# Kernel optimization log

Hardware: AMD Instinct MI355X
Metric: run time of the kernel (lower is better)

The kernel has to match this reference:

```python
import jax, jax.numpy as jnp
import numpy as np

W_DIM = 72  # positional_encoding(3 coords, 12 freqs) -> 3*12*2
_F1 = np.array([1.0, 3.0, 3.0, 1.0], dtype=np.float32)
_F2 = np.outer(_F1, _F1); _F2 = _F2 / _F2.sum()  # normalized StyleGAN resample filter


def upsample2x(x):
    """Antialiased 2x upsample: zero-insertion + 4-tap [1,3,3,1] FIR, gain=4 (upfirdn2d)."""
    C = x.shape[1]
    k = jnp.tile(jnp.asarray(_F2 * 4.0, x.dtype)[None, None], (C, 1, 1, 1))  # [C,1,4,4]
    return jax.lax.conv_general_dilated(
        x, k, (1, 1), ((2, 2), (2, 2)), lhs_dilation=(2, 2),
        feature_group_count=C, dimension_numbers=('NCHW', 'OIHW', 'NCHW'))


def affine(w_vec, aw, ab):
    # FullyConnectedLayer: runtime weight gain 1/sqrt(w_dim), bias init 1
    return (w_vec @ aw.T) / np.sqrt(W_DIM) + ab


def mod_conv(x, weight, styles, demodulate=True, padding=1):
    """StyleGAN2 modulated conv2d (batch=1). weight [Co,Ci,k,k], styles [Ci]."""
    w = weight * styles[None, :, None, None]
    if demodulate:
        d = jax.lax.rsqrt(jnp.sum(w * w, axis=(1, 2, 3)) + 1e-8)
        w = w * d[:, None, None, None]
    return jax.lax.conv_general_dilated(
        x, w, (1, 1), ((padding, padding), (padding, padding)),
        dimension_numbers=('NCHW', 'OIHW', 'NCHW'))


def syn_layer(x, w_vec, aw, ab, cw, cb, up):
    s = affine(w_vec, aw, ab)
    if up:
        x = upsample2x(x)
    x = mod_conv(x, cw, s, True, 1)
    # bias_act: lrelu, gain sqrt(2), conv_clamp 256 (noise_strength init 0 -> no noise)
    x = jax.nn.leaky_relu(x + cb[None, :, None, None], 0.2) * np.sqrt(2.0)
    return jnp.clip(x, -256.0, 256.0)


def to_rgb(x, w_vec, aw, ab, cw, cb):
    s = affine(w_vec, aw, ab) / np.sqrt(cw.shape[1])  # ToRGB weight_gain 1/sqrt(Cin)
    y = mod_conv(x, cw, s, False, 0)
    return jnp.clip(y + cb[None, :, None, None], -256.0, 256.0)


def reference(rays, rgbs, conv_w, conv_b, bn_gamma, bn_beta, bn_mean, bn_var,
              a0_w, a0_b, w0, b0, a1_w, a1_b, w1, b1, t0_aw, t0_ab, t0_w, t0_b,
              a2_w, a2_b, w2, b2, a3_w, a3_b, w3, b3, t1_aw, t1_ab, t1_w, t1_b):
    # style vector from positional encoding of ray origin
    p = rays[0, :3, 0, 0]
    fb = 2.0 ** jnp.arange(12, dtype=rays.dtype)
    pts = (p[:, None] * fb[None, :]).reshape(-1)  # (36,)
    w_vec = jnp.concatenate([jnp.sin(pts), jnp.cos(pts)])  # (72,)
    # mapping: 1x1 conv + relu + BatchNorm2d (eval-mode)
    feat = jnp.einsum('oi,bihw->bohw', conv_w[:, :, 0, 0], rgbs) + conv_b[None, :, None, None]
    feat = jax.nn.relu(feat)
    inv = jax.lax.rsqrt(bn_var + 1e-5)
    feat = (feat - bn_mean[None, :, None, None]) * (inv * bn_gamma)[None, :, None, None] + bn_beta[None, :, None, None]
    rgb = feat[:, :3]
    # block0: 32ch@128 -> 256ch@256, skip-architecture ToRGB
    x = syn_layer(feat, w_vec, a0_w, a0_b, w0, b0, True)
    x = syn_layer(x, w_vec, a1_w, a1_b, w1, b1, False)
    img = upsample2x(rgb) + to_rgb(x, w_vec, t0_aw, t0_ab, t0_w, t0_b)
    # block1: 256ch@256 -> 128ch@512
    x = syn_layer(x, w_vec, a2_w, a2_b, w2, b2, True)
    x = syn_layer(x, w_vec, a3_w, a3_b, w3, b3, False)
    img = upsample2x(img) + to_rgb(x, w_vec, t1_aw, t1_ab, t1_w, t1_b)
    return img  # [1,3,512,512]


def setup_inputs() -> dict:
    key = jax.random.key(0)
    ks = jax.random.split(key, 16)
    rn = lambda k, s: jax.random.normal(k, s, dtype=jnp.float32)
    z = lambda s: jnp.zeros(s, jnp.float32)
    o = lambda s: jnp.ones(s, jnp.float32)
    inp = {}
    inp['rays'] = rn(ks[0], (1, 6, 128, 128))
    inp['rgbs'] = jax.random.uniform(ks[1], (1, 3, 128, 128), dtype=jnp.float32)
    inp['conv_w'] = rn(ks[2], (32, 3, 1, 1)); inp['conv_b'] = z((32,))
    inp['bn_gamma'] = o((32,)); inp['bn_beta'] = z((32,))
    inp['bn_mean'] = z((32,)); inp['bn_var'] = o((32,))
    inp['a0_w'] = rn(ks[3], (32, 72)); inp['a0_b'] = o((32,))
    inp['w0'] = rn(ks[4], (256, 32, 3, 3)); inp['b0'] = z((256,))
    inp['a1_w'] = rn(ks[5], (256, 72)); inp['a1_b'] = o((256,))
    inp['w1'] = rn(ks[6], (256, 256, 3, 3)); inp['b1'] = z((256,))
    inp['t0_aw'] = rn(ks[7], (256, 72)); inp['t0_ab'] = o((256,))
    inp['t0_w'] = rn(ks[8], (3, 256, 1, 1)); inp['t0_b'] = z((3,))
    inp['a2_w'] = rn(ks[9], (256, 72)); inp['a2_b'] = o((256,))
    inp['w2'] = rn(ks[10], (128, 256, 3, 3)); inp['b2'] = z((128,))
    inp['a3_w'] = rn(ks[11], (128, 72)); inp['a3_b'] = o((128,))
    inp['w3'] = rn(ks[12], (128, 128, 3, 3)); inp['b3'] = z((128,))
    inp['t1_aw'] = rn(ks[13], (128, 72)); inp['t1_ab'] = o((128,))
    inp['t1_w'] = rn(ks[14], (3, 128, 1, 1)); inp['t1_b'] = z((3,))
    return inp
```

## Files before the change

### kernel.cpp

```cpp
#include <hip/hip_runtime.h>
#include <cstddef>

typedef __attribute__((ext_vector_type(8))) short short8;
typedef __attribute__((ext_vector_type(4))) float f32x4;
typedef __attribute__((address_space(3))) void lds_void;
typedef const __attribute__((address_space(1))) void glob_void;

static const size_t OFF_S0    = 0;
static const size_t OFF_S1    = 64;
static const size_t OFF_S2    = 320;
static const size_t OFF_S3    = 576;
static const size_t OFF_MT0   = 704;
static const size_t OFF_MT1   = 1472;
static const size_t OFF_ZERO  = 1856;
static const size_t OFF_RGBF  = 2048;
static const size_t OFF_IMG0  = 51200;
static const size_t OFF_RGBP  = 247808;
static const size_t OFF_WQ0   = 1900544;
static const size_t OFF_WQ1   = 1937408;
static const size_t OFF_WQ2   = 2232320;
static const size_t OFF_WQ3   = 2379776;
static const size_t OFF_FEAT  = 2453504;
static const size_t OFF_UFEAT = 2715648;
static const size_t OFF_X1    = 4194304;
static const size_t OFF_X2    = 4194304;
static const size_t OFF_U     = 20971520;
static const size_t OFF_X0    = 20971520;

__device__ __forceinline__ unsigned short f2bf(float f) {
  unsigned int u = __float_as_uint(f);
  return (unsigned short)((u + 0x7FFFu + ((u >> 16) & 1u)) >> 16);
}
__device__ __forceinline__ float b2f(short h) {
  return __uint_as_float(((unsigned int)(unsigned short)h) << 16);
}

__global__ void __launch_bounds__(256) prep_kernel(
    const float* __restrict__ rays,
    const float* __restrict__ a0w, const float* __restrict__ a0b,
    const float* __restrict__ a1w, const float* __restrict__ a1b,
    const float* __restrict__ t0aw, const float* __restrict__ t0ab,
    const float* __restrict__ a2w, const float* __restrict__ a2b,
    const float* __restrict__ a3w, const float* __restrict__ a3b,
    const float* __restrict__ t1aw, const float* __restrict__ t1ab,
    const float* __restrict__ t0w, const float* __restrict__ t1w,
    float* __restrict__ ws)
{
  __shared__ float wv[72];
  __shared__ float st0l[256];
  __shared__ float st1l[128];
  const int tid = threadIdx.x;
  if (tid < 128) ws[OFF_ZERO + tid] = 0.f;
  if (tid < 36) {
    int i = tid / 12, j = tid % 12;
    float v = rays[i * 16384] * (float)(1 << j);
    wv[tid]      = sinf(v);
    wv[36 + tid] = cosf(v);
  }
  __syncthreads();
  const float inv72 = 0.11785113019775793f;

  if (tid < 32) {
    float d = 0.f;
    for (int k = 0; k < 72; ++k) d += wv[k] * a0w[tid * 72 + k];
    ws[OFF_S0 + tid] = fmaf(d, inv72, a0b[tid]);
  }
  {
    float d = 0.f;
    for (int k = 0; k < 72; ++k) d += wv[k] * a1w[tid * 72 + k];
    ws[OFF_S1 + tid] = fmaf(d, inv72, a1b[tid]);
  }
  {
    float d = 0.f;
    for (int k = 0; k < 72; ++k) d += wv[k] * t0aw[tid * 72 + k];
    st0l[tid] = fmaf(d, inv72, t0ab[tid]) * 0.0625f;
  }
  {
    float d = 0.f;
    for (int k = 0; k < 72; ++k) d += wv[k] * a2w[tid * 72 + k];
    ws[OFF_S2 + tid] = fmaf(d, inv72, a2b[tid]);
  }
  if (tid < 128) {
    float d = 0.f;
    for (int k = 0; k < 72; ++k) d += wv[k] * a3w[tid * 72 + k];
    ws[OFF_S3 + tid] = fmaf(d, inv72, a3b[tid]);
  }
  if (tid < 128) {
    float d = 0.f;
    for (int k = 0; k < 72; ++k) d += wv[k] * t1aw[tid * 72 + k];
    st1l[tid] = fmaf(d, inv72, t1ab[tid]) * 0.08838834764831845f;
  }
  __syncthreads();
  for (int i = tid; i < 768; i += 256) ws[OFF_MT0 + i] = t0w[i] * st0l[i & 255];
  for (int i = tid; i < 384; i += 256) ws[OFF_MT1 + i] = t1w[i] * st1l[i & 127];
}

__global__ void __launch_bounds__(256) modw_kernel(
    const float* __restrict__ w, const float* __restrict__ s,
    unsigned short* __restrict__ wq, int Ci, int Co)
{
  const int co = blockIdx.x;
  const int n = Ci * 9;
  float local = 0.f;
  for (int i = threadIdx.x; i < n; i += 256) {
    float v = w[co * n + i] * s[i / 9];
    local += v * v;
  }
#pragma unroll
  for (int off = 32; off >= 1; off >>= 1) local += __shfl_xor(local, off);
  __shared__ float red[4];
  if ((threadIdx.x & 63) == 0) red[threadIdx.x >> 6] = local;
  __syncthreads();
  const float d = rsqrtf(red[0] + red[1] + red[2] + red[3] + 1e-8f);
  for (int i = threadIdx.x; i < n; i += 256) {
    int ci = i / 9, t = i - ci * 9;
    wq[(((size_t)(ci >> 5) * 9 + t) * Co + co) * 32 + (ci & 31)] =
        f2bf(w[co * n + i] * s[ci] * d);
  }
}

__global__ void __launch_bounds__(256) feat_kernel(
    const float* __restrict__ rgbs, const float* __restrict__ cw, const float* __restrict__ cb,
    const float* __restrict__ gam, const float* __restrict__ bet,
    const float* __restrict__ mean, const float* __restrict__ var,
    unsigned short* __restrict__ feat, float* __restrict__ rgbf)
{
  const int p = blockIdx.x * 256 + threadIdx.x;
  const float r = rgbs[p], g = rgbs[16384 + p], b = rgbs[32768 + p];
  unsigned int pk[16];
#pragma unroll
  for (int co = 0; co < 32; ++co) {
    float v = cw[co * 3] * r + cw[co * 3 + 1] * g + cw[co * 3 + 2] * b + cb[co];
    v = fmaxf(v, 0.f);
    float inv = rsqrtf(var[co] + 1e-5f);
    v = (v - mean[co]) * (inv * gam[co]) + bet[co];
    if (co < 3) rgbf[co * 16384 + p] = v;
    unsigned int h = f2bf(v);
    if ((co & 1) == 0) pk[co >> 1] = h;
    else               pk[co >> 1] |= h << 16;
  }
  uint4* dst = reinterpret_cast<uint4*>(feat + (size_t)p * 32);
#pragma unroll
  for (int q = 0; q < 4; ++q)
    dst[q] = make_uint4(pk[q * 4], pk[q * 4 + 1], pk[q * 4 + 2], pk[q * 4 + 3]);
}

__global__ void __launch_bounds__(256) up2x_nhwc_kernel(
    const unsigned short* __restrict__ in, unsigned short* __restrict__ out,
    int H, int W, int c8s , int w2s )
{
  const int cid = blockIdx.x * 256 + threadIdx.x;
  const int k = cid & ((1 << c8s) - 1);
  const int pix = cid >> c8s;
  const int ey = pix >> w2s;
  const int ex = pix & ((1 << w2s) - 1);
  const int C = 8 << c8s;
  int ry0; float ay0, ay1;
  if (ey & 1) { ry0 = ey >> 1;       ay0 = 0.75f; ay1 = 0.25f; }
  else        { ry0 = (ey >> 1) - 1; ay0 = 0.25f; ay1 = 0.75f; }
  int cx0; float bx0, bx1;
  if (ex & 1) { cx0 = ex >> 1;       bx0 = 0.75f; bx1 = 0.25f; }
  else        { cx0 = (ex >> 1) - 1; bx0 = 0.25f; bx1 = 0.75f; }
  const short8 z = {0, 0, 0, 0, 0, 0, 0, 0};
  short8 v00 = z, v01 = z, v10 = z, v11 = z;
  const bool yo0 = (ry0 >= 0), yo1 = (ry0 + 1 < H);
  const bool xo0 = (cx0 >= 0), xo1 = (cx0 + 1 < W);
  if (yo0 && xo0) v00 = *reinterpret_cast<const short8*>(in + ((size_t)(ry0 * W + cx0) * C + k * 8));
  if (yo0 && xo1) v01 = *reinterpret_cast<const short8*>(in + ((size_t)(ry0 * W + cx0 + 1) * C + k * 8));
  if (yo1 && xo0) v10 = *reinterpret_cast<const short8*>(in + ((size_t)((ry0 + 1) * W + cx0) * C + k * 8));
  if (yo1 && xo1) v11 = *reinterpret_cast<const short8*>(in + ((size_t)((ry0 + 1) * W + cx0 + 1) * C + k * 8));
  unsigned int o[4];
#pragma unroll
  for (int j = 0; j < 8; ++j) {
    float f = ay0 * (bx0 * b2f(v00[j]) + bx1 * b2f(v01[j]))
            + ay1 * (bx0 * b2f(v10[j]) + bx1 * b2f(v11[j]));
    unsigned int h = f2bf(f);
    if ((j & 1) == 0) o[j >> 1] = h;
    else              o[j >> 1] |= h << 16;
  }
  *reinterpret_cast<uint4*>(out + (size_t)pix * C + k * 8) = make_uint4(o[0], o[1], o[2], o[3]);
}

template <bool FUSE_RGB>
__global__ void __launch_bounds__(512) conv3x3_mfma(
    const unsigned short* __restrict__ in,
    const unsigned short* __restrict__ wq,
    const float* __restrict__ bias,
    unsigned short* __restrict__ out,
    const float* __restrict__ rgbw,
    float* __restrict__ rgbp,
    const unsigned short* __restrict__ zpage,
    int H, int W, int Ci, int Co)
{
  const int tid  = threadIdx.x;
  const int lane = tid & 63;
  const int wv   = tid >> 6;
  const int wr   = wv & 3;
  const int wg   = wv >> 2;
  const int lo   = lane & 15, hi = lane >> 4;
  const int tpr  = W >> 4;
  const int T_y  = (blockIdx.x / tpr) << 4;
  const int T_x  = (blockIdx.x % tpr) << 4;
  const int cog  = (blockIdx.y * 2 + wg) << 6;

  __shared__ short8 xs[2][1296];
  __shared__ float  rw[FUSE_RGB ? 384 : 4];

  if (FUSE_RGB) {
    for (int i = tid; i < 3 * Co; i += 512) rw[i] = rgbw[i];
  }

  f32x4 acc[4][4];
#pragma unroll
  for (int a = 0; a < 4; ++a)
#pragma unroll
    for (int b = 0; b < 4; ++b) acc[a][b] = (f32x4){0.f, 0.f, 0.f, 0.f};

  const unsigned short* gsrc[3];
#pragma unroll
  for (int j = 0; j < 3; ++j) {
    const int s = j * 512 + tid;
    const int pix = s >> 2, kslot = s & 3;
    const int rr = pix / 18, cc = pix - rr * 18;
    const int gy = T_y - 1 + rr, gx = T_x - 1 + cc;
    const int k = kslot ^ ((cc >> 1) & 3);
    const bool inb = (s < 1296) && gy >= 0 && gy < H && gx >= 0 && gx < W;
    gsrc[j] = inb ? (in + ((size_t)(gy * W + gx) * Ci + (k << 3))) : zpage;
  }

#define STAGE(c, buf)                                                              \
  {                                                                                \
    const int cb_ = (c) << 5;                                                      \
    _Pragma("unroll")                                                              \
    for (int j = 0; j < 2; ++j)                                                    \
      __builtin_amdgcn_global_load_lds((glob_void*)(gsrc[j] + cb_),                \
                                       (lds_void*)&xs[buf][j * 512 + tid], 16, 0, 0); \
    if (tid < 272)                                                                 \
      __builtin_amdgcn_global_load_lds((glob_void*)(gsrc[2] + cb_),                \
                                       (lds_void*)&xs[buf][1024 + tid], 16, 0, 0); \
  }

  const int nch = Ci >> 5;
  const int nsteps = nch * 9;
  const unsigned short* wa = wq + ((size_t)(cog + lo) << 5) + (hi << 3);
  const int wstride = Co << 5;
  short8 apf[3][4];

#define ALOAD(SLOT, STEP)                                                          \
  {                                                                                \
    const unsigned short* wp_ = wa + (size_t)(STEP) * wstride;                     \
    _Pragma("unroll")                                                              \
    for (int cf = 0; cf < 4; ++cf)                                                 \
      apf[SLOT][cf] = *reinterpret_cast<const short8*>(wp_ + (cf << 9));           \
  }

  STAGE(0, 0);
  ALOAD(0, 0);
  ALOAD(1, 1);
  __syncthreads();

  for (int c = 0; c < nch; ++c) {
    const int cur = c & 1;
    if (c + 1 < nch) STAGE(c + 1, cur ^ 1);

    const int pbase = c * 9;
#pragma unroll
    for (int tap = 0; tap < 9; ++tap) {
      const int ky = tap / 3, kx = tap - (tap / 3) * 3;
      const int pstep = pbase + tap + 2;
      if (pstep < nsteps) ALOAD((tap + 2) % 3, pstep);
#pragma unroll
      for (int r = 0; r < 4; ++r) {
        const int trow = (wr << 2) + r + ky;
        const int tx2  = lo + kx;
        const int pix  = trow * 18 + tx2;
        const short8 b = xs[cur][(pix << 2) + (hi ^ ((tx2 >> 1) & 3))];
#pragma unroll
        for (int cf = 0; cf < 4; ++cf)
          acc[cf][r] = __builtin_amdgcn_mfma_f32_16x16x32_bf16(apf[tap % 3][cf], b,
                                                               acc[cf][r], 0, 0, 0);
      }
    }
    __syncthreads();
  }
#undef STAGE
#undef ALOAD

  const float rt2 = 1.41421356237309515f;
#pragma unroll
  for (int r = 0; r < 4; ++r) {
    const int gy = T_y + (wr << 2) + r;
    const int gx = T_x + lo;
    if (!FUSE_RGB) {
#pragma unroll
      for (int cf = 0; cf < 4; ++cf) {
        const int cb = cog + (cf << 4) + (hi << 2);
        const f32x4 bi = *reinterpret_cast<const f32x4*>(bias + cb);
        unsigned short h[4];
#pragma unroll
        for (int reg = 0; reg < 4; ++reg) {
          float vv = acc[cf][r][reg] + bi[reg];
          vv = (vv >= 0.f) ? vv : 0.2f * vv;
          vv *= rt2;
          vv = fminf(fmaxf(vv, -256.f), 256.f);
          h[reg] = f2bf(vv);
        }
        uint2 pk;
        pk.x = (unsigned int)h[0] | ((unsigned int)h[1] << 16);
        pk.y = (unsigned int)h[2] | ((unsigned int)h[3] << 16);
        *reinterpret_cast<uint2*>(out + (size_t)(gy * W + gx) * Co + cb) = pk;
      }
    } else {
      float p0 = 0.f, p1 = 0.f, p2 = 0.f;
#pragma unroll
      for (int cf = 0; cf < 4; ++cf) {
        const int cb = cog + (cf << 4) + (hi << 2);
        const f32x4 bi = *reinterpret_cast<const f32x4*>(bias + cb);
#pragma unroll
        for (int reg = 0; reg < 4; ++reg) {
          float vv = acc[cf][r][reg] + bi[reg];
          vv = (vv >= 0.f) ? vv : 0.2f * vv;
          vv *= rt2;
          vv = fminf(fmaxf(vv, -256.f), 256.f);
          p0 = fmaf(rw[cb + reg], vv, p0);
          p1 = fmaf(rw[Co + cb + reg], vv, p1);
          p2 = fmaf(rw[2 * Co + cb + reg], vv, p2);
        }
      }
      p0 += __shfl_xor(p0, 16); p0 += __shfl_xor(p0, 32);
      p1 += __shfl_xor(p1, 16); p1 += __shfl_xor(p1, 32);
      p2 += __shfl_xor(p2, 16); p2 += __shfl_xor(p2, 32);
      if (hi == 0) {
        const size_t HWs = (size_t)H * W;
        const size_t px  = (size_t)gy * W + gx;
        rgbp[((size_t)wg * 3 + 0) * HWs + px] = p0;
        rgbp[((size_t)wg * 3 + 1) * HWs + px] = p1;
        rgbp[((size_t)wg * 3 + 2) * HWs + px] = p2;
      }
    }
  }
}

__device__ __forceinline__ float up2x_sample(const float* __restrict__ im, int H, int W,
                                             int oy, int ox)
{
  int my = oy >> 1, mx = ox >> 1;
  int ry0; float ay0, ay1;
  if (oy & 1) { ry0 = my;     ay0 = 0.75f; ay1 = 0.25f; }
  else        { ry0 = my - 1; ay0 = 0.25f; ay1 = 0.75f; }
  int cx0; float bx0, bx1;
  if (ox & 1) { cx0 = mx;     bx0 = 0.75f; bx1 = 0.25f; }
  else        { cx0 = mx - 1; bx0 = 0.25f; bx1 = 0.75f; }
  float v00 = (ry0 >= 0    && cx0 >= 0   ) ? im[ry0 * W + cx0]           : 0.f;
  float v01 = (ry0 >= 0    && cx0 + 1 < W) ? im[ry0 * W + cx0 + 1]       : 0.f;
  float v10 = (ry0 + 1 < H && cx0 >= 0   ) ? im[(ry0 + 1) * W + cx0]     : 0.f;
  float v11 = (ry0 + 1 < H && cx0 + 1 < W) ? im[(ry0 + 1) * W + cx0 + 1] : 0.f;
  return ay0 * (bx0 * v00 + bx1 * v01) + ay1 * (bx0 * v10 + bx1 * v11);
}

__global__ void __launch_bounds__(256) img0_kernel(
    const float* __restrict__ rgbf, const unsigned short* __restrict__ x1,
    const float* __restrict__ mt0g, const float* __restrict__ tb,
    float* __restrict__ img0)
{
  __shared__ float mt[768];
  const int tid = threadIdx.x;
  for (int i = tid; i < 768; i += 256) mt[i] = mt0g[i];
  __syncthreads();
  const int p = blockIdx.x * 256 + tid;
  const unsigned short* xp = x1 + (size_t)p * 256;
  float a0 = 0.f, a1 = 0.f, a2 = 0.f;
  for (int i8 = 0; i8 < 32; ++i8) {
    const short8 v = *reinterpret_cast<const short8*>(xp + i8 * 8);
#pragma unroll
    for (int j = 0; j < 8; ++j) {
      const float xv = b2f(v[j]);
      const int ci = i8 * 8 + j;
      a0 = fmaf(mt[ci],       xv, a0);
      a1 = fmaf(mt[256 + ci], xv, a1);
      a2 = fmaf(mt[512 + ci], xv, a2);
    }
  }
  const int oy = p >> 8, ox = p & 255;
  float av[3] = {a0, a1, a2};
#pragma unroll
  for (int o = 0; o < 3; ++o) {
    float y = fminf(fmaxf(av[o] + tb[o], -256.f), 256.f);
    img0[o * 65536 + p] = up2x_sample(rgbf + o * 16384, 128, 128, oy, ox) + y;
  }
}

__global__ void __launch_bounds__(256) final_kernel(
    const float* __restrict__ img0, const float* __restrict__ rgbp,
    const float* __restrict__ tb, float* __restrict__ out)
{
  const int p = blockIdx.x * 256 + threadIdx.x;
  const int oy = p >> 9, ox = p & 511;
#pragma unroll
  for (int o = 0; o < 3; ++o) {
    float a = rgbp[(0 * 3 + o) * 262144 + p] + rgbp[(1 * 3 + o) * 262144 + p];
    float y = fminf(fmaxf(a + tb[o], -256.f), 256.f);
    out[o * 262144 + p] = up2x_sample(img0 + o * 65536, 256, 256, oy, ox) + y;
  }
}

extern "C" void kernel_launch(void* const* d_in, const int* in_sizes, int n_in,
                              void* d_out, int out_size, void* d_ws, size_t ws_size,
                              hipStream_t stream)
{
  const float* rays   = (const float*)d_in[0];
  const float* rgbs   = (const float*)d_in[1];
  const float* conv_w = (const float*)d_in[2];
  const float* conv_b = (const float*)d_in[3];
  const float* bn_g   = (const float*)d_in[4];
  const float* bn_b   = (const float*)d_in[5];
  const float* bn_m   = (const float*)d_in[6];
  const float* bn_v   = (const float*)d_in[7];
  const float* a0_w   = (const float*)d_in[8];
  const float* a0_b   = (const float*)d_in[9];
  const float* w0     = (const float*)d_in[10];
  const float* b0     = (const float*)d_in[11];
  const float* a1_w   = (const float*)d_in[12];
  const float* a1_b   = (const float*)d_in[13];
  const float* w1     = (const float*)d_in[14];
  const float* b1     = (const float*)d_in[15];
  const float* t0_aw  = (const float*)d_in[16];
  const float* t0_ab  = (const float*)d_in[17];
  const float* t0_w   = (const float*)d_in[18];
  const float* t0_b   = (const float*)d_in[19];
  const float* a2_w   = (const float*)d_in[20];
  const float* a2_b   = (const float*)d_in[21];
  const float* w2     = (const float*)d_in[22];
  const float* b2     = (const float*)d_in[23];
  const float* a3_w   = (const float*)d_in[24];
  const float* a3_b   = (const float*)d_in[25];
  const float* w3     = (const float*)d_in[26];
  const float* b3     = (const float*)d_in[27];
  const float* t1_aw  = (const float*)d_in[28];
  const float* t1_ab  = (const float*)d_in[29];
  const float* t1_w   = (const float*)d_in[30];
  const float* t1_b   = (const float*)d_in[31];

  float* ws  = (float*)d_ws;
  float* out = (float*)d_out;

  unsigned short* wq0   = (unsigned short*)(ws + OFF_WQ0);
  unsigned short* wq1   = (unsigned short*)(ws + OFF_WQ1);
  unsigned short* wq2   = (unsigned short*)(ws + OFF_WQ2);
  unsigned short* wq3   = (unsigned short*)(ws + OFF_WQ3);
  unsigned short* featb = (unsigned short*)(ws + OFF_FEAT);
  unsigned short* ufeat = (unsigned short*)(ws + OFF_UFEAT);
  unsigned short* x0b   = (unsigned short*)(ws + OFF_X0);
  unsigned short* x1b   = (unsigned short*)(ws + OFF_X1);
  unsigned short* x2b   = (unsigned short*)(ws + OFF_X2);
  unsigned short* Ub    = (unsigned short*)(ws + OFF_U);
  const unsigned short* zpage = (const unsigned short*)(ws + OFF_ZERO);

  prep_kernel<<<1, 256, 0, stream>>>(rays, a0_w, a0_b, a1_w, a1_b, t0_aw, t0_ab,
                                     a2_w, a2_b, a3_w, a3_b, t1_aw, t1_ab,
                                     t0_w, t1_w, ws);
  modw_kernel<<<256, 256, 0, stream>>>(w0, ws + OFF_S0, wq0, 32, 256);
  modw_kernel<<<256, 256, 0, stream>>>(w1, ws + OFF_S1, wq1, 256, 256);
  modw_kernel<<<128, 256, 0, stream>>>(w2, ws + OFF_S2, wq2, 256, 128);
  modw_kernel<<<128, 256, 0, stream>>>(w3, ws + OFF_S3, wq3, 128, 128);
  feat_kernel<<<64, 256, 0, stream>>>(rgbs, conv_w, conv_b, bn_g, bn_b, bn_m, bn_v,
                                      featb, ws + OFF_RGBF);
  up2x_nhwc_kernel<<<1024, 256, 0, stream>>>(featb, ufeat, 128, 128, 2, 8);
  conv3x3_mfma<false><<<dim3(256, 2), 512, 0, stream>>>(
      ufeat, wq0, b0, x0b, nullptr, nullptr, zpage, 256, 256, 32, 256);
  conv3x3_mfma<false><<<dim3(256, 2), 512, 0, stream>>>(
      x0b, wq1, b1, x1b, nullptr, nullptr, zpage, 256, 256, 256, 256);
  img0_kernel<<<256, 256, 0, stream>>>(ws + OFF_RGBF, x1b, ws + OFF_MT0, t0_b,
                                       ws + OFF_IMG0);
  up2x_nhwc_kernel<<<32768, 256, 0, stream>>>(x1b, Ub, 256, 256, 5, 9);
  conv3x3_mfma<false><<<dim3(1024, 1), 512, 0, stream>>>(
      Ub, wq2, b2, x2b, nullptr, nullptr, zpage, 512, 512, 256, 128);
  conv3x3_mfma<true><<<dim3(1024, 1), 512, 0, stream>>>(
      x2b, wq3, b3, nullptr, ws + OFF_MT1, ws + OFF_RGBP, zpage, 512, 512, 128, 128);
  final_kernel<<<1024, 256, 0, stream>>>(ws + OFF_IMG0, ws + OFF_RGBP, t1_b, out);
}
```

Measured before the change: 488.8 us.

## Switch conv3x3 to 32x32x16 MFMA with 64-channel blocks and new LDS swizzle

Reworks the 3x3 conv kernel to use 32x32x16 bf16 MFMA instructions. Each wave now covers a 2x16 pixel strip against 64 output channels, and each block handles 64 output channels, so grid.y doubles. The LDS swizzle gains a row-parity XOR to avoid bank conflicts under the new access pattern. The aim is higher MFMA throughput per instruction and less per-lane LDS traffic. The cost is that each input tile is now loaded by twice as many blocks, and the rgb partial sums are indexed by blockIdx.y, which must stay consistent with how final_kernel reduces them.

Result: slower. 975.7 us (+99.6%).

```diff
diff --git a/kernel.cpp b/kernel.cpp
--- a/kernel.cpp
+++ b/kernel.cpp
@@ -3,6 +3,7 @@
 
 typedef __attribute__((ext_vector_type(8))) short short8;
 typedef __attribute__((ext_vector_type(4))) float f32x4;
+typedef __attribute__((ext_vector_type(16))) float f32x16;
 typedef __attribute__((address_space(3))) void lds_void;
 typedef const __attribute__((address_space(1))) void glob_void;
 
@@ -195,13 +196,13 @@
   const int tid  = threadIdx.x;
   const int lane = tid & 63;
   const int wv   = tid >> 6;
-  const int wr   = wv & 3;
-  const int wg   = wv >> 2;
-  const int lo   = lane & 15, hi = lane >> 4;
+  const int px   = lane & 31;
+  const int hi5  = lane >> 5;
+  const int prow = px >> 4, pcol = px & 15;
   const int tpr  = W >> 4;
   const int T_y  = (blockIdx.x / tpr) << 4;
   const int T_x  = (blockIdx.x % tpr) << 4;
-  const int cog  = (blockIdx.y * 2 + wg) << 6;
+  const int cog  = blockIdx.y << 6;
 
   __shared__ short8 xs[2][1296];
   __shared__ float  rw[FUSE_RGB ? 384 : 4];
@@ -210,11 +211,9 @@
     for (int i = tid; i < 3 * Co; i += 512) rw[i] = rgbw[i];
   }
 
-  f32x4 acc[4][4];
-#pragma unroll
-  for (int a = 0; a < 4; ++a)
-#pragma unroll
-    for (int b = 0; b < 4; ++b) acc[a][b] = (f32x4){0.f, 0.f, 0.f, 0.f};
+  f32x16 acc0 = {0.f}, acc1 = {0.f};
+#pragma unroll
+  for (int i = 0; i < 16; ++i) { acc0[i] = 0.f; acc1[i] = 0.f; }
 
   const unsigned short* gsrc[3];
 #pragma unroll
@@ -223,7 +222,7 @@
     const int pix = s >> 2, kslot = s & 3;
     const int rr = pix / 18, cc = pix - rr * 18;
     const int gy = T_y - 1 + rr, gx = T_x - 1 + cc;
-    const int k = kslot ^ ((cc >> 1) & 3);
+    const int k = kslot ^ ((cc >> 1) & 3) ^ ((rr & 1) << 1);
     const bool inb = (s < 1296) && gy >= 0 && gy < H && gx >= 0 && gx < W;
     gsrc[j] = inb ? (in + ((size_t)(gy * W + gx) * Ci + (k << 3))) : zpage;
   }
@@ -241,17 +240,16 @@
   }
 
   const int nch = Ci >> 5;
-  const int nsteps = nch * 9;
-  const unsigned short* wa = wq + ((size_t)(cog + lo) << 5) + (hi << 3);
-  const int wstride = Co << 5;
-  short8 apf[3][4];
-
-#define ALOAD(SLOT, STEP)                                                          \
+  const int nsteps2 = nch * 18;
+  const unsigned short* wa = wq + ((size_t)(cog + px) << 5) + (hi5 << 3);
+  const size_t wstride = (size_t)Co << 5;
+  short8 apf[3][2];
+
+#define ALOAD(SLOT, G)                                                             \
   {                                                                                \
-    const unsigned short* wp_ = wa + (size_t)(STEP) * wstride;                     \
-    _Pragma("unroll")                                                              \
-    for (int cf = 0; cf < 4; ++cf)                                                 \
-      apf[SLOT][cf] = *reinterpret_cast<const short8*>(wp_ + (cf << 9));           \
+    const unsigned short* wp_ = wa + (size_t)((G) >> 1) * wstride + (((G) & 1) << 4); \
+    apf[SLOT][0] = *reinterpret_cast<const short8*>(wp_);                          \
+    apf[SLOT][1] = *reinterpret_cast<const short8*>(wp_ + 1024);                   \
   }
 
   STAGE(0, 0);
@@ -263,22 +261,21 @@
     const int cur = c & 1;
     if (c + 1 < nch) STAGE(c + 1, cur ^ 1);
 
-    const int pbase = c * 9;
+    const int base2 = c * 18;
 #pragma unroll
     for (int tap = 0; tap < 9; ++tap) {
       const int ky = tap / 3, kx = tap - (tap / 3) * 3;
-      const int pstep = pbase + tap + 2;
-      if (pstep < nsteps) ALOAD((tap + 2) % 3, pstep);
-#pragma unroll
-      for (int r = 0; r < 4; ++r) {
-        const int trow = (wr << 2) + r + ky;
-        const int tx2  = lo + kx;
-        const int pix  = trow * 18 + tx2;
-        const short8 b = xs[cur][(pix << 2) + (hi ^ ((tx2 >> 1) & 3))];
-#pragma unroll
-        for (int cf = 0; cf < 4; ++cf)
-          acc[cf][r] = __builtin_amdgcn_mfma_f32_16x16x32_bf16(apf[tap % 3][cf], b,
-                                                               acc[cf][r], 0, 0, 0);
+      const int trow = (wv << 1) + prow + ky;
+      const int tcol = pcol + kx;
+      const int pixb = (trow * 18 + tcol) << 2;
+      const int sxor = ((tcol >> 1) & 3) ^ ((trow & 1) << 1);
+#pragma unroll
+      for (int ks = 0; ks < 2; ++ks) {
+        const int gstep = base2 + tap * 2 + ks + 2;
+        if (gstep < nsteps2) ALOAD((tap * 2 + ks + 2) % 3, gstep);
+        const short8 b = xs[cur][pixb + (((ks << 1) + hi5) ^ sxor)];
+        acc0 = __builtin_amdgcn_mfma_f32_32x32x16_bf16(apf[(tap * 2 + ks) % 3][0], b, acc0, 0, 0, 0);
+        acc1 = __builtin_amdgcn_mfma_f32_32x32x16_bf16(apf[(tap * 2 + ks) % 3][1], b, acc1, 0, 0, 0);
       }
     }
     __syncthreads();
@@ -287,56 +284,59 @@
 #undef ALOAD
 
   const float rt2 = 1.41421356237309515f;
-#pragma unroll
-  for (int r = 0; r < 4; ++r) {
-    const int gy = T_y + (wr << 2) + r;
-    const int gx = T_x + lo;
-    if (!FUSE_RGB) {
-#pragma unroll
-      for (int cf = 0; cf < 4; ++cf) {
-        const int cb = cog + (cf << 4) + (hi << 2);
+  const int gy = T_y + (wv << 1) + prow;
+  const int gx = T_x + pcol;
+  if (!FUSE_RGB) {
+#pragma unroll
+    for (int ct = 0; ct < 2; ++ct) {
+#pragma unroll
+      for (int q = 0; q < 4; ++q) {
+        const int cb = cog + (ct << 5) + (q << 3) + (hi5 << 2);
         const f32x4 bi = *reinterpret_cast<const f32x4*>(bias + cb);
         unsigned short h[4];
 #pragma unroll
-        for (int reg = 0; reg < 4; ++reg) {
-          float vv = acc[cf][r][reg] + bi[reg];
+        for (int i = 0; i < 4; ++i) {
+          float vv = (ct == 0 ? acc0[q * 4 + i] : acc1[q * 4 + i]) + bi[i];
           vv = (vv >= 0.f) ? vv : 0.2f * vv;
           vv *= rt2;
           vv = fminf(fmaxf(vv, -256.f), 256.f);
-          h[reg] = f2bf(vv);
+          h[i] = f2bf(vv);
         }
         uint2 pk;
         pk.x = (unsigned int)h[0] | ((unsigned int)h[1] << 16);
         pk.y = (unsigned int)h[2] | ((unsigned int)h[3] << 16);
         *reinterpret_cast<uint2*>(out + (size_t)(gy * W + gx) * Co + cb) = pk;
       }
-    } else {
-      float p0 = 0.f, p1 = 0.f, p2 = 0.f;
-#pragma unroll
-      for (int cf = 0; cf < 4; ++cf) {
-        const int cb = cog + (cf << 4) + (hi << 2);
+    }
+  } else {
+    float p0 = 0.f, p1 = 0.f, p2 = 0.f;
+#pragma unroll
+    for (int ct = 0; ct < 2; ++ct) {
+#pragma unroll
+      for (int q = 0; q < 4; ++q) {
+        const int cb = cog + (ct << 5) + (q << 3) + (hi5 << 2);
         const f32x4 bi = *reinterpret_cast<const f32x4*>(bias + cb);
 #pragma unroll
-        for (int reg = 0; reg < 4; ++reg) {
-          float vv = acc[cf][r][reg] + bi[reg];
+        for (int i = 0; i < 4; ++i) {
+          float vv = (ct == 0 ? acc0[q * 4 + i] : acc1[q * 4 + i]) + bi[i];
           vv = (vv >= 0.f) ? vv : 0.2f * vv;
           vv *= rt2;
           vv = fminf(fmaxf(vv, -256.f), 256.f);
-          p0 = fmaf(rw[cb + reg], vv, p0);
-          p1 = fmaf(rw[Co + cb + reg], vv, p1);
-          p2 = fmaf(rw[2 * Co + cb + reg], vv, p2);
+          p0 = fmaf(rw[cb + i], vv, p0);
+          p1 = fmaf(rw[Co + cb + i], vv, p1);
+          p2 = fmaf(rw[2 * Co + cb + i], vv, p2);
         }
       }
-      p0 += __shfl_xor(p0, 16); p0 += __shfl_xor(p0, 32);
-      p1 += __shfl_xor(p1, 16); p1 += __shfl_xor(p1, 32);
-      p2 += __shfl_xor(p2, 16); p2 += __shfl_xor(p2, 32);
-      if (hi == 0) {
-        const size_t HWs = (size_t)H * W;
-        const size_t px  = (size_t)gy * W + gx;
-        rgbp[((size_t)wg * 3 + 0) * HWs + px] = p0;
-        rgbp[((size_t)wg * 3 + 1) * HWs + px] = p1;
-        rgbp[((size_t)wg * 3 + 2) * HWs + px] = p2;
-      }
+    }
+    p0 += __shfl_xor(p0, 32);
+    p1 += __shfl_xor(p1, 32);
+    p2 += __shfl_xor(p2, 32);
+    if (hi5 == 0) {
+      const size_t HWs = (size_t)H * W;
+      const size_t pxi = (size_t)gy * W + gx;
+      rgbp[((size_t)blockIdx.y * 3 + 0) * HWs + pxi] = p0;
+      rgbp[((size_t)blockIdx.y * 3 + 1) * HWs + pxi] = p1;
+      rgbp[((size_t)blockIdx.y * 3 + 2) * HWs + pxi] = p2;
     }
   }
 }
@@ -466,16 +466,16 @@
   feat_kernel<<<64, 256, 0, stream>>>(rgbs, conv_w, conv_b, bn_g, bn_b, bn_m, bn_v,
                                       featb, ws + OFF_RGBF);
   up2x_nhwc_kernel<<<1024, 256, 0, stream>>>(featb, ufeat, 128, 128, 2, 8);
-  conv3x3_mfma<false><<<dim3(256, 2), 512, 0, stream>>>(
+  conv3x3_mfma<false><<<dim3(256, 4), 512, 0, stream>>>(
       ufeat, wq0, b0, x0b, nullptr, nullptr, zpage, 256, 256, 32, 256);
-  conv3x3_mfma<false><<<dim3(256, 2), 512, 0, stream>>>(
+  conv3x3_mfma<false><<<dim3(256, 4), 512, 0, stream>>>(
       x0b, wq1, b1, x1b, nullptr, nullptr, zpage, 256, 256, 256, 256);
   img0_kernel<<<256, 256, 0, stream>>>(ws + OFF_RGBF, x1b, ws + OFF_MT0, t0_b,
                                        ws + OFF_IMG0);
   up2x_nhwc_kernel<<<32768, 256, 0, stream>>>(x1b, Ub, 256, 256, 5, 9);
-  conv3x3_mfma<false><<<dim3(1024, 1), 512, 0, stream>>>(
+  conv3x3_mfma<false><<<dim3(1024, 2), 512, 0, stream>>>(
       Ub, wq2, b2, x2b, nullptr, nullptr, zpage, 512, 512, 256, 128);
-  conv3x3_mfma<true><<<dim3(1024, 1), 512, 0, stream>>>(
+  conv3x3_mfma<true><<<dim3(1024, 2), 512, 0, stream>>>(
       x2b, wq3, b3, nullptr, ws + OFF_MT1, ws + OFF_RGBP, zpage, 512, 512, 128, 128);
   final_kernel<<<1024, 256, 0, stream>>>(ws + OFF_IMG0, ws + OFF_RGBP, t1_b, out);
 }
```
